# Optimization experiments

Hardware: AMD Instinct MI355X
Metric: run time of the kernel (lower is better)

## Reference

```python
import jax, jax.numpy as jnp
import numpy as np

B, S, D, M = 4, 1024, 128, 20000
THRESH = 0.1          # memory.query_with_indices threshold
CW_MIN = 0.01         # compound_weight > 0.01 gate
TI_MIN = 0.01         # total_influence > 0.01 gate
NORM_EPS = 1e-6       # norm_sq > 1e-6 gate
INF_EPS = 1e-5        # division epsilon


def setup_inputs() -> dict:
    key = jax.random.key(0)
    ks = jax.random.split(key, 4)
    sd = 1.0 / np.sqrt(D)
    return {
        "input_tensor": jax.random.normal(ks[0], (B, S, D), dtype=jnp.float32),
        "mem": jax.random.normal(ks[1], (M, D), dtype=jnp.float32),
        "W1": jax.random.normal(ks[2], (D, D), dtype=jnp.float32) * sd,
        "b1": jnp.zeros((D,), dtype=jnp.float32),
        "ln_g": jnp.ones((D,), dtype=jnp.float32),
        "ln_b": jnp.zeros((D,), dtype=jnp.float32),
        "W2": jax.random.normal(ks[3], (D, D), dtype=jnp.float32) * sd,
        "b2": jnp.zeros((D,), dtype=jnp.float32),
    }


def reference(input_tensor, mem, W1, b1, ln_g, ln_b, W2, b2):
    x = input_tensor  # [B,S,D]
    # fusion_net: Linear -> LayerNorm -> ReLU
    h = jnp.einsum("bsd,ed->bse", x, W1) + b1
    mu = h.mean(-1, keepdims=True)
    var = h.var(-1, keepdims=True)
    h = (h - mu) * jax.lax.rsqrt(var + 1e-5) * ln_g + ln_b
    feats = jax.nn.relu(h)
    raw = jnp.einsum("bsd,ed->bse", feats, W2) + b2  # [B,S,D]

    # GraphMemory query: cosine similarity, keep entries with sim > THRESH
    xn = x * jax.lax.rsqrt(jnp.sum(x * x, -1, keepdims=True) + 1e-12)
    mn = mem * jax.lax.rsqrt(jnp.sum(mem * mem, -1, keepdims=True) + 1e-12)
    sim = jnp.einsum("bsd,md->bsm", xn, mn)              # [B,S,M]
    w = jnp.where(sim > THRESH, sim, 0.0)                # per-token weights

    # compound_weight per batch & memory slot (sum over seq positions)
    cw = w.sum(axis=1)                                   # [B,M]
    norm_sq = jnp.sum(mem * mem, -1)                     # [M]
    active = (cw > CW_MIN) & (norm_sq > NORM_EPS)        # [B,M]
    eff = jnp.where(active, cw, 0.0)                     # effective weights

    # projection of each target vec onto each memory vec
    safe_ns = jnp.where(norm_sq > NORM_EPS, norm_sq, 1.0)
    coef = jnp.einsum("bsd,md->bsm", raw, mem) / safe_ns # [B,S,M]
    correction = jnp.einsum("bsm,bm,md->bsd", coef, eff, mem)  # [B,S,D]

    ti = eff.sum(-1)                                     # [B] total_influence
    corr = correction / (ti + INF_EPS)[:, None, None]
    final = jnp.where((ti > TI_MIN)[:, None, None], raw + 0.5 * corr, raw)
    return final
```

## Files before the change

### kernel.cpp

```cpp
#include <hip/hip_runtime.h>

#define DD 128
#define SS 1024
#define BB 4
#define M_TOT 20000
#define M_PAD 20480
#define GM_NCH 64
#define GM_CH 320
#define FMLP_BLOCKS 128
#define PREP_BLOCKS 320

typedef __bf16 bf16x8 __attribute__((ext_vector_type(8)));
typedef _Float16 f16x8 __attribute__((ext_vector_type(8)));
typedef unsigned short u16x8 __attribute__((ext_vector_type(8)));
typedef float f32x16 __attribute__((ext_vector_type(16)));

union BF8 { bf16x8 b; u16x8 u; };

__device__ __forceinline__ unsigned short f2bf(float f) {
    __bf16 h = (__bf16)f;
    return __builtin_bit_cast(unsigned short, h);
}
__device__ __forceinline__ float bf2f(unsigned short h) {
    return __uint_as_float(((unsigned int)h) << 16);
}

__global__ __launch_bounds__(256) void k_front(
    const float* __restrict__ x, const float* __restrict__ W1,
    const float* __restrict__ b1, const float* __restrict__ ln_g,
    const float* __restrict__ ln_b, const float* __restrict__ W2,
    const float* __restrict__ b2, const float* __restrict__ mem,
    unsigned short* __restrict__ xnb, float* __restrict__ raw,
    unsigned short* __restrict__ mnb, _Float16* __restrict__ mnT,
    float* __restrict__ norm_sq, float* __restrict__ ti,
    float* __restrict__ cw, float* __restrict__ G) {
    __shared__ __align__(16) char smem_raw[64 * 136 * 2];
    const int tid = threadIdx.x;
    const int bid = blockIdx.x;

    if (bid < FMLP_BLOCKS) {
        unsigned short* featsL = (unsigned short*)smem_raw;
        float* redp = (float*)(smem_raw + 8704);
        float2* stats = (float2*)(smem_raw + 8704 + 1024);
        const int lane = tid & 63, wv = tid >> 6;
        const int col = lane & 31, hi = lane >> 5;
        const int t0 = bid * 32;
        const int ct = wv;

        bf16x8 Af[8];
        float sq = 0.f;
        const float* xrow = x + (size_t)(t0 + col) * DD + hi * 8;
        #pragma unroll
        for (int kk = 0; kk < 8; ++kk) {
            float4 p = *(const float4*)(xrow + kk * 16);
            float4 q = *(const float4*)(xrow + kk * 16 + 4);
            BF8 t;
            t.u[0] = f2bf(p.x); t.u[1] = f2bf(p.y); t.u[2] = f2bf(p.z); t.u[3] = f2bf(p.w);
            t.u[4] = f2bf(q.x); t.u[5] = f2bf(q.y); t.u[6] = f2bf(q.z); t.u[7] = f2bf(q.w);
            Af[kk] = t.b;
            sq += p.x * p.x + p.y * p.y + p.z * p.z + p.w * p.w;
            sq += q.x * q.x + q.y * q.y + q.z * q.z + q.w * q.w;
        }
        sq += __shfl_xor(sq, 32);
        float xrs = rsqrtf(sq + 1e-12f);
        if (wv == 0) {
            unsigned short* xo = xnb + (size_t)(t0 + col) * DD + hi * 8;
            #pragma unroll
            for (int kk = 0; kk < 8; ++kk) {
                BF8 t; t.b = Af[kk];
                u16x8 o;
                #pragma unroll
                for (int j = 0; j < 8; ++j) o[j] = f2bf(bf2f(t.u[j]) * xrs);
                *(u16x8*)(xo + kk * 16) = o;
            }
        }

        f32x16 acc;
        {
            float bv = b1[ct * 32 + col];
            #pragma unroll
            for (int r = 0; r < 16; ++r) acc[r] = bv;
        }
        const float* w1row = W1 + (size_t)(ct * 32 + col) * DD + hi * 8;
        #pragma unroll
        for (int kk = 0; kk < 8; ++kk) {
            float4 p = *(const float4*)(w1row + kk * 16);
            float4 q = *(const float4*)(w1row + kk * 16 + 4);
            BF8 t;
            t.u[0] = f2bf(p.x); t.u[1] = f2bf(p.y); t.u[2] = f2bf(p.z); t.u[3] = f2bf(p.w);
            t.u[4] = f2bf(q.x); t.u[5] = f2bf(q.y); t.u[6] = f2bf(q.z); t.u[7] = f2bf(q.w);
            acc = __builtin_amdgcn_mfma_f32_32x32x16_bf16(Af[kk], t.b, acc, 0, 0, 0);
        }

        float rs_[16], rq_[16];
        #pragma unroll
        for (int r = 0; r < 16; ++r) { float v = acc[r]; rs_[r] = v; rq_[r] = v * v; }
        #pragma unroll
        for (int off = 1; off < 32; off <<= 1) {
            #pragma unroll
            for (int r = 0; r < 16; ++r) {
                rs_[r] += __shfl_xor(rs_[r], off);
                rq_[r] += __shfl_xor(rq_[r], off);
            }
        }
        if (col == 0) {
            #pragma unroll
            for (int r = 0; r < 16; ++r) {
                int row = (r & 3) + 8 * (r >> 2) + 4 * hi;
                redp[(wv * 32 + row) * 2 + 0] = rs_[r];
                redp[(wv * 32 + row) * 2 + 1] = rq_[r];
            }
        }
        __syncthreads();
        if (tid < 32) {
            float S = redp[(0 * 32 + tid) * 2] + redp[(1 * 32 + tid) * 2] +
                      redp[(2 * 32 + tid) * 2] + redp[(3 * 32 + tid) * 2];
            float Q = redp[(0 * 32 + tid) * 2 + 1] + redp[(1 * 32 + tid) * 2 + 1] +
                      redp[(2 * 32 + tid) * 2 + 1] + redp[(3 * 32 + tid) * 2 + 1];
            float mu = S * (1.f / 128.f);
            float rstd = rsqrtf(Q * (1.f / 128.f) - mu * mu + 1e-5f);
            stats[tid] = make_float2(mu, rstd);
        }
        __syncthreads();

        {
            float gv = ln_g[ct * 32 + col], bv = ln_b[ct * 32 + col];
            #pragma unroll
            for (int r = 0; r < 16; ++r) {
                int row = (r & 3) + 8 * (r >> 2) + 4 * hi;
                float2 st = stats[row];
                float v = fmaxf((acc[r] - st.x) * st.y * gv + bv, 0.f);
                featsL[row * 136 + ct * 32 + col] = f2bf(v);
            }
        }
        __syncthreads();

        f32x16 a2;
        {
            float bv = b2[ct * 32 + col];
            #pragma unroll
            for (int r = 0; r < 16; ++r) a2[r] = bv;
        }
        const float* w2row = W2 + (size_t)(ct * 32 + col) * DD + hi * 8;
        #pragma unroll
        for (int kk = 0; kk < 8; ++kk) {
            bf16x8 Aq = *(const bf16x8*)&featsL[(lane & 31) * 136 + hi * 8 + kk * 16];
            float4 p = *(const float4*)(w2row + kk * 16);
            float4 q = *(const float4*)(w2row + kk * 16 + 4);
            BF8 t;
            t.u[0] = f2bf(p.x); t.u[1] = f2bf(p.y); t.u[2] = f2bf(p.z); t.u[3] = f2bf(p.w);
            t.u[4] = f2bf(q.x); t.u[5] = f2bf(q.y); t.u[6] = f2bf(q.z); t.u[7] = f2bf(q.w);
            a2 = __builtin_amdgcn_mfma_f32_32x32x16_bf16(Aq, t.b, a2, 0, 0, 0);
        }
        #pragma unroll
        for (int r = 0; r < 16; ++r) {
            int row = (r & 3) + 8 * (r >> 2) + 4 * hi;
            raw[(size_t)(t0 + row) * DD + ct * 32 + col] = a2[r];
        }
    } else {
        unsigned short* RM = (unsigned short*)smem_raw;
        const int pb = bid - FMLP_BLOCKS;
        const int m0 = pb * 64;
        cw[pb * 256 + tid] = 0.0f;
        if (pb < 64) ((float4*)G)[pb * 256 + tid] =
            make_float4(0.f, 0.f, 0.f, 0.f);
        if (pb == 0 && tid < BB) ti[tid] = 0.0f;

        const int r = tid >> 2, seg = tid & 3;
        const int m = m0 + r;
        const bool ok = m < M_TOT;
        float4 v[8];
        const float4* src = (const float4*)mem + (size_t)m * 32 + seg * 8;
        #pragma unroll
        for (int i = 0; i < 8; ++i)
            v[i] = ok ? src[i] : make_float4(0.f, 0.f, 0.f, 0.f);
        float ss = 0.f;
        #pragma unroll
        for (int i = 0; i < 8; ++i)
            ss += v[i].x * v[i].x + v[i].y * v[i].y + v[i].z * v[i].z + v[i].w * v[i].w;
        ss += __shfl_xor(ss, 1);
        ss += __shfl_xor(ss, 2);
        float rs = rsqrtf(ss + 1e-12f);
        if (seg == 0) norm_sq[m] = ss;

        #pragma unroll
        for (int i = 0; i < 4; ++i) {
            float4 a = v[2 * i], bq = v[2 * i + 1];
            u16x8 o;
            o[0] = f2bf(a.x * rs); o[1] = f2bf(a.y * rs);
            o[2] = f2bf(a.z * rs); o[3] = f2bf(a.w * rs);
            o[4] = f2bf(bq.x * rs); o[5] = f2bf(bq.y * rs);
            o[6] = f2bf(bq.z * rs); o[7] = f2bf(bq.w * rs);
            *(u16x8*)(mnb + (size_t)m * DD + seg * 32 + i * 8) = o;
            *(u16x8*)(RM + r * 136 + seg * 32 + i * 8) = o;
        }
        __syncthreads();
        const int d = tid >> 1, half = tid & 1;
        _Float16* dst = mnT + (size_t)d * M_PAD + m0 + half * 32;
        #pragma unroll
        for (int q = 0; q < 4; ++q) {
            f16x8 o;
            #pragma unroll
            for (int j = 0; j < 8; ++j)
                o[j] = (_Float16)bf2f(RM[(half * 32 + q * 8 + j) * 136 + d]);
            *(f16x8*)(dst + q * 8) = o;
        }
    }
}

__global__ __launch_bounds__(256, 3) void k_cw(
    const unsigned short* __restrict__ xnb, const unsigned short* __restrict__ mnb,
    float* __restrict__ cw) {
    __shared__ unsigned short As[4][32 * 128];
    const int tid = threadIdx.x, lane = tid & 63, wv = tid >> 6;
    const int c = lane & 31, h = lane >> 5;
    const int b = blockIdx.z;
    const int mw = blockIdx.x * 256 + wv * 64;
    const int s_base = blockIdx.y * 256;

    const int srow = tid >> 4, sk16 = tid & 15;
    const int soff = srow * 128 + ((sk16 * 8) ^ ((srow & 15) << 3));
    const int srow1 = srow + 16;
    const int soff1 = srow1 * 128 + ((sk16 * 8) ^ ((srow1 & 15) << 3));
    const unsigned short* xbase = xnb + ((size_t)b * SS + s_base) * DD;

    bf16x8 Bf[2][8];
    #pragma unroll
    for (int ct = 0; ct < 2; ++ct)
        #pragma unroll
        for (int kk = 0; kk < 8; ++kk)
            Bf[ct][kk] = *(const bf16x8*)(mnb + (size_t)(mw + ct * 32 + c) * DD +
                                          kk * 16 + h * 8);

    {
        u16x8 a0 = *(const u16x8*)(xbase + (size_t)srow * DD + sk16 * 8);
        u16x8 a1 = *(const u16x8*)(xbase + (size_t)srow1 * DD + sk16 * 8);
        const unsigned short* n1 = xbase + (size_t)32 * DD;
        u16x8 b0 = *(const u16x8*)(n1 + (size_t)srow * DD + sk16 * 8);
        u16x8 b1 = *(const u16x8*)(n1 + (size_t)srow1 * DD + sk16 * 8);
        *(u16x8*)&As[0][soff] = a0; *(u16x8*)&As[0][soff1] = a1;
        *(u16x8*)&As[1][soff] = b0; *(u16x8*)&As[1][soff1] = b1;
    }

    float cw0 = 0.f, cw1 = 0.f;
    #pragma unroll 1
    for (int p = 0; p < 4; ++p) {
        __syncthreads();
        u16x8 w0, w1, w2, w3;
        if (p < 3) {
            const unsigned short* n0 = xbase + (size_t)(2 * p + 2) * 32 * DD;
            const unsigned short* n1 = xbase + (size_t)(2 * p + 3) * 32 * DD;
            w0 = *(const u16x8*)(n0 + (size_t)srow * DD + sk16 * 8);
            w1 = *(const u16x8*)(n0 + (size_t)srow1 * DD + sk16 * 8);
            w2 = *(const u16x8*)(n1 + (size_t)srow * DD + sk16 * 8);
            w3 = *(const u16x8*)(n1 + (size_t)srow1 * DD + sk16 * 8);
        }
        {
            f32x16 p0, p1;
            #pragma unroll
            for (int r = 0; r < 16; ++r) { p0[r] = 0.f; p1[r] = 0.f; }
            const unsigned short* Ab = As[(2 * p) & 3];
            __builtin_amdgcn_s_setprio(1);
            #pragma unroll
            for (int kk = 0; kk < 8; ++kk) {
                bf16x8 Afr = *(const bf16x8*)&Ab[c * 128 + ((kk * 16 + h * 8) ^ ((c & 15) << 3))];
                p0 = __builtin_amdgcn_mfma_f32_32x32x16_bf16(Afr, Bf[0][kk], p0, 0, 0, 0);
                p1 = __builtin_amdgcn_mfma_f32_32x32x16_bf16(Afr, Bf[1][kk], p1, 0, 0, 0);
            }
            __builtin_amdgcn_s_setprio(0);
            #pragma unroll
            for (int r = 0; r < 16; ++r) {
                float a = p0[r], bb = p1[r];
                cw0 += a > 0.1f ? a : 0.f;
                cw1 += bb > 0.1f ? bb : 0.f;
            }
        }
        {
            f32x16 p0, p1;
            #pragma unroll
            for (int r = 0; r < 16; ++r) { p0[r] = 0.f; p1[r] = 0.f; }
            const unsigned short* Ab = As[(2 * p + 1) & 3];
            __builtin_amdgcn_s_setprio(1);
            #pragma unroll
            for (int kk = 0; kk < 8; ++kk) {
                bf16x8 Afr = *(const bf16x8*)&Ab[c * 128 + ((kk * 16 + h * 8) ^ ((c & 15) << 3))];
                p0 = __builtin_amdgcn_mfma_f32_32x32x16_bf16(Afr, Bf[0][kk], p0, 0, 0, 0);
                p1 = __builtin_amdgcn_mfma_f32_32x32x16_bf16(Afr, Bf[1][kk], p1, 0, 0, 0);
            }
            __builtin_amdgcn_s_setprio(0);
            if (p < 3) {
                unsigned short* An0 = As[(2 * p + 2) & 3];
                unsigned short* An1 = As[(2 * p + 3) & 3];
                *(u16x8*)&An0[soff] = w0; *(u16x8*)&An0[soff1] = w1;
                *(u16x8*)&An1[soff] = w2; *(u16x8*)&An1[soff1] = w3;
            }
            #pragma unroll
            for (int r = 0; r < 16; ++r) {
                float a = p0[r], bb = p1[r];
                cw0 += a > 0.1f ? a : 0.f;
                cw1 += bb > 0.1f ? bb : 0.f;
            }
        }
    }
    cw0 += __shfl_xor(cw0, 32);
    cw1 += __shfl_xor(cw1, 32);
    if (lane < 32) {
        atomicAdd(&cw[(size_t)b * M_PAD + mw + c], cw0);
        atomicAdd(&cw[(size_t)b * M_PAD + mw + 32 + c], cw1);
    }
}

__global__ __launch_bounds__(256) void k_gmatm(
    const _Float16* __restrict__ mnT, const float* __restrict__ cw,
    const float* __restrict__ norm_sq, float* __restrict__ ti,
    float* __restrict__ G) {
    __shared__ __align__(16) _Float16 effH[GM_CH];
    __shared__ float rb[4];
    const int tid = threadIdx.x, lane = tid & 63, wv = tid >> 6;
    const int c = lane & 31, h = lane >> 5;
    const int b = blockIdx.y;
    const int m0 = blockIdx.x * GM_CH;

    float tsum = 0.f;
    #pragma unroll
    for (int idx = tid; idx < GM_CH; idx += 256) {
        int m = m0 + idx;
        float e = 0.f;
        if (m < M_TOT) {
            float cc = cw[(size_t)b * M_PAD + m];
            float ns = norm_sq[m];
            e = (cc > 0.01f && ns > 1e-6f) ? cc : 0.f;
        }
        effH[idx] = (_Float16)e;
        tsum += e;
    }
    #pragma unroll
    for (int off = 1; off < 64; off <<= 1) tsum += __shfl_xor(tsum, off);
    if (lane == 0) rb[wv] = tsum;
    __syncthreads();
    if (tid == 0) atomicAdd(&ti[b], rb[0] + rb[1] + rb[2] + rb[3]);

    f32x16 a0, a1, a2, a3;
    #pragma unroll
    for (int r = 0; r < 16; ++r) { a0[r] = 0.f; a1[r] = 0.f; a2[r] = 0.f; a3[r] = 0.f; }

    const _Float16* Arow = mnT + (size_t)(wv * 32 + c) * M_PAD + m0;
    const _Float16* B0r = mnT + (size_t)(0 * 32 + c) * M_PAD + m0;
    const _Float16* B1r = mnT + (size_t)(1 * 32 + c) * M_PAD + m0;
    const _Float16* B2r = mnT + (size_t)(2 * 32 + c) * M_PAD + m0;
    const _Float16* B3r = mnT + (size_t)(3 * 32 + c) * M_PAD + m0;

    #pragma unroll 1
    for (int t = 0; t < GM_CH / 64; ++t) {
        #pragma unroll
        for (int kk = 0; kk < 4; ++kk) {
            const int mo = t * 64 + kk * 16 + h * 8;
            f16x8 au = *(const f16x8*)(Arow + mo);
            f16x8 ef = *(const f16x8*)&effH[mo];
            f16x8 af = au * ef;
            f16x8 B0 = *(const f16x8*)(B0r + mo);
            f16x8 B1 = *(const f16x8*)(B1r + mo);
            f16x8 B2 = *(const f16x8*)(B2r + mo);
            f16x8 B3 = *(const f16x8*)(B3r + mo);
            a0 = __builtin_amdgcn_mfma_f32_32x32x16_f16(af, B0, a0, 0, 0, 0);
            a1 = __builtin_amdgcn_mfma_f32_32x32x16_f16(af, B1, a1, 0, 0, 0);
            a2 = __builtin_amdgcn_mfma_f32_32x32x16_f16(af, B2, a2, 0, 0, 0);
            a3 = __builtin_amdgcn_mfma_f32_32x32x16_f16(af, B3, a3, 0, 0, 0);
        }
    }
    float* Gb = G + (size_t)b * DD * DD;
    #pragma unroll
    for (int r = 0; r < 16; ++r) {
        int rf = (r & 3) + 8 * (r >> 2) + 4 * h;
        atomicAdd(&Gb[(wv * 32 + rf) * DD + 0 * 32 + c], a0[r]);
        atomicAdd(&Gb[(wv * 32 + rf) * DD + 1 * 32 + c], a1[r]);
        atomicAdd(&Gb[(wv * 32 + rf) * DD + 2 * 32 + c], a2[r]);
        atomicAdd(&Gb[(wv * 32 + rf) * DD + 3 * 32 + c], a3[r]);
    }
}

__global__ __launch_bounds__(256) void k_final(
    const float* __restrict__ raw, const float* __restrict__ G,
    const float* __restrict__ ti, float* __restrict__ out) {
    const int tid = threadIdx.x, lane = tid & 63, wv = tid >> 6;
    const int col = lane & 31, hi = lane >> 5;
    const int t0 = blockIdx.x * 32;
    const int b = blockIdx.x >> 5;
    const int ct = wv;

    bf16x8 Af[8];
    const float* rrow = raw + (size_t)(t0 + col) * DD + hi * 8;
    #pragma unroll
    for (int kk = 0; kk < 8; ++kk) {
        float4 p = *(const float4*)(rrow + kk * 16);
        float4 q = *(const float4*)(rrow + kk * 16 + 4);
        BF8 t;
        t.u[0] = f2bf(p.x); t.u[1] = f2bf(p.y); t.u[2] = f2bf(p.z); t.u[3] = f2bf(p.w);
        t.u[4] = f2bf(q.x); t.u[5] = f2bf(q.y); t.u[6] = f2bf(q.z); t.u[7] = f2bf(q.w);
        Af[kk] = t.b;
    }
    f32x16 acc;
    #pragma unroll
    for (int r = 0; r < 16; ++r) acc[r] = 0.f;
    const float* grow = G + (size_t)b * DD * DD + (size_t)(ct * 32 + col) * DD + hi * 8;
    #pragma unroll
    for (int kk = 0; kk < 8; ++kk) {
        float4 p = *(const float4*)(grow + kk * 16);
        float4 q = *(const float4*)(grow + kk * 16 + 4);
        BF8 t;
        t.u[0] = f2bf(p.x); t.u[1] = f2bf(p.y); t.u[2] = f2bf(p.z); t.u[3] = f2bf(p.w);
        t.u[4] = f2bf(q.x); t.u[5] = f2bf(q.y); t.u[6] = f2bf(q.z); t.u[7] = f2bf(q.w);
        acc = __builtin_amdgcn_mfma_f32_32x32x16_bf16(Af[kk], t.b, acc, 0, 0, 0);
    }
    float tib = ti[b];
    float scale = (tib > 0.01f) ? 0.5f / (tib + 1e-5f) : 0.0f;
    #pragma unroll
    for (int r = 0; r < 16; ++r) {
        int row = (r & 3) + 8 * (r >> 2) + 4 * hi;
        size_t idx = (size_t)(t0 + row) * DD + ct * 32 + col;
        out[idx] = raw[idx] + scale * acc[r];
    }
}

extern "C" void kernel_launch(void* const* d_in, const int* in_sizes, int n_in,
                              void* d_out, int out_size, void* d_ws, size_t ws_size,
                              hipStream_t stream) {
    const float* x   = (const float*)d_in[0];
    const float* mem = (const float*)d_in[1];
    const float* W1  = (const float*)d_in[2];
    const float* b1  = (const float*)d_in[3];
    const float* lg  = (const float*)d_in[4];
    const float* lb  = (const float*)d_in[5];
    const float* W2  = (const float*)d_in[6];
    const float* b2  = (const float*)d_in[7];
    float* out = (float*)d_out;

    float* wsf = (float*)d_ws;
    size_t off = 0;
    unsigned short* mnb = (unsigned short*)(wsf + off); off += (size_t)M_PAD * 64;
    _Float16* mnT = (_Float16*)(wsf + off);             off += (size_t)M_PAD * 64;
    float* norm_sq = wsf + off;                         off += M_PAD;
    unsigned short* xnb = (unsigned short*)(wsf + off); off += (size_t)BB * SS * 64;
    float* raw = wsf + off;                             off += (size_t)BB * SS * DD;
    float* cw  = wsf + off;                             off += (size_t)BB * M_PAD;
    float* G   = wsf + off;                             off += (size_t)BB * DD * DD;
    float* ti  = wsf + off;                             off += BB;

    k_front<<<dim3(FMLP_BLOCKS + PREP_BLOCKS), 256, 0, stream>>>(
        x, W1, b1, lg, lb, W2, b2, mem, xnb, raw, mnb, mnT, norm_sq, ti, cw, G);
    k_cw<<<dim3(M_PAD / 256, 4, BB), 256, 0, stream>>>(xnb, mnb, cw);
    k_gmatm<<<dim3(GM_NCH, BB), 256, 0, stream>>>(mnT, cw, norm_sq, ti, G);
    k_final<<<dim3(SS * BB / 32), 256, 0, stream>>>(raw, G, ti, out);
}
```

Baseline: 83.96 us.

## Replace G atomic accumulation with per-chunk partials and a separate reduction kernel

k_gmatm now writes each chunk's 128x128 partial Gram matrix to its own slot instead of issuing float atomics into a shared G. A new kernel k_gmat2 sums the 64 partials per batch and stores G as bf16, so k_final loads bf16 directly without converting. The aim is to remove contention from the atomic adds and the G zero-init in k_front. The cost is an extra launch and about 16 MB of partial-buffer writes and reads.

```diff
diff --git a/kernel.cpp b/kernel.cpp
--- a/kernel.cpp
+++ b/kernel.cpp
@@ -33,7 +33,7 @@
     unsigned short* __restrict__ xnb, float* __restrict__ raw,
     unsigned short* __restrict__ mnb, _Float16* __restrict__ mnT,
     float* __restrict__ norm_sq, float* __restrict__ ti,
-    float* __restrict__ cw, float* __restrict__ G) {
+    float* __restrict__ cw) {
     __shared__ __align__(16) char smem_raw[64 * 136 * 2];
     const int tid = threadIdx.x;
     const int bid = blockIdx.x;
@@ -162,8 +162,6 @@
         const int pb = bid - FMLP_BLOCKS;
         const int m0 = pb * 64;
         cw[pb * 256 + tid] = 0.0f;
-        if (pb < 64) ((float4*)G)[pb * 256 + tid] =
-            make_float4(0.f, 0.f, 0.f, 0.f);
         if (pb == 0 && tid < BB) ti[tid] = 0.0f;
 
         const int r = tid >> 2, seg = tid & 3;
@@ -313,7 +311,7 @@
 __global__ __launch_bounds__(256) void k_gmatm(
     const _Float16* __restrict__ mnT, const float* __restrict__ cw,
     const float* __restrict__ norm_sq, float* __restrict__ ti,
-    float* __restrict__ G) {
+    float* __restrict__ pG) {
     __shared__ __align__(16) _Float16 effH[GM_CH];
     __shared__ float rb[4];
     const int tid = threadIdx.x, lane = tid & 63, wv = tid >> 6;
@@ -368,19 +366,45 @@
             a3 = __builtin_amdgcn_mfma_f32_32x32x16_f16(af, B3, a3, 0, 0, 0);
         }
     }
-    float* Gb = G + (size_t)b * DD * DD;
+    float* o = pG + (size_t)(blockIdx.x * BB + b) * (DD * DD);
     #pragma unroll
     for (int r = 0; r < 16; ++r) {
         int rf = (r & 3) + 8 * (r >> 2) + 4 * h;
-        atomicAdd(&Gb[(wv * 32 + rf) * DD + 0 * 32 + c], a0[r]);
-        atomicAdd(&Gb[(wv * 32 + rf) * DD + 1 * 32 + c], a1[r]);
-        atomicAdd(&Gb[(wv * 32 + rf) * DD + 2 * 32 + c], a2[r]);
-        atomicAdd(&Gb[(wv * 32 + rf) * DD + 3 * 32 + c], a3[r]);
+        o[(wv * 32 + rf) * DD + 0 * 32 + c] = a0[r];
+        o[(wv * 32 + rf) * DD + 1 * 32 + c] = a1[r];
+        o[(wv * 32 + rf) * DD + 2 * 32 + c] = a2[r];
+        o[(wv * 32 + rf) * DD + 3 * 32 + c] = a3[r];
+    }
+}
+
+__global__ __launch_bounds__(256) void k_gmat2(const float* __restrict__ pG,
+                                               unsigned short* __restrict__ Gb) {
+    __shared__ float4 redv[256];
+    const int tid = threadIdx.x;
+    const int b = blockIdx.y;
+    const int f4i = blockIdx.x * 64 + (tid & 63);
+    const int cg = tid >> 6;
+    const float4* pG4 = (const float4*)pG;
+    float4 s = make_float4(0.f, 0.f, 0.f, 0.f);
+    for (int c = cg; c < GM_NCH; c += 4) {
+        float4 p = pG4[(size_t)(c * BB + b) * (DD * DD / 4) + f4i];
+        s.x += p.x; s.y += p.y; s.z += p.z; s.w += p.w;
+    }
+    redv[tid] = s;
+    __syncthreads();
+    if (tid < 64) {
+        float4 r0 = redv[tid], r1 = redv[tid + 64], r2 = redv[tid + 128], r3 = redv[tid + 192];
+        ushort4 o;
+        o.x = f2bf(r0.x + r1.x + r2.x + r3.x);
+        o.y = f2bf(r0.y + r1.y + r2.y + r3.y);
+        o.z = f2bf(r0.z + r1.z + r2.z + r3.z);
+        o.w = f2bf(r0.w + r1.w + r2.w + r3.w);
+        *(ushort4*)&Gb[(size_t)b * (DD * DD) + f4i * 4] = o;
     }
 }
 
 __global__ __launch_bounds__(256) void k_final(
-    const float* __restrict__ raw, const float* __restrict__ G,
+    const float* __restrict__ raw, const unsigned short* __restrict__ Gb,
     const float* __restrict__ ti, float* __restrict__ out) {
     const int tid = threadIdx.x, lane = tid & 63, wv = tid >> 6;
     const int col = lane & 31, hi = lane >> 5;
@@ -402,15 +426,11 @@
     f32x16 acc;
     #pragma unroll
     for (int r = 0; r < 16; ++r) acc[r] = 0.f;
-    const float* grow = G + (size_t)b * DD * DD + (size_t)(ct * 32 + col) * DD + hi * 8;
+    const unsigned short* grow = Gb + (size_t)b * DD * DD + (size_t)(ct * 32 + col) * DD + hi * 8;
     #pragma unroll
     for (int kk = 0; kk < 8; ++kk) {
-        float4 p = *(const float4*)(grow + kk * 16);
-        float4 q = *(const float4*)(grow + kk * 16 + 4);
-        BF8 t;
-        t.u[0] = f2bf(p.x); t.u[1] = f2bf(p.y); t.u[2] = f2bf(p.z); t.u[3] = f2bf(p.w);
-        t.u[4] = f2bf(q.x); t.u[5] = f2bf(q.y); t.u[6] = f2bf(q.z); t.u[7] = f2bf(q.w);
-        acc = __builtin_amdgcn_mfma_f32_32x32x16_bf16(Af[kk], t.b, acc, 0, 0, 0);
+        bf16x8 Bw = *(const bf16x8*)(grow + kk * 16);
+        acc = __builtin_amdgcn_mfma_f32_32x32x16_bf16(Af[kk], Bw, acc, 0, 0, 0);
     }
     float tib = ti[b];
     float scale = (tib > 0.01f) ? 0.5f / (tib + 1e-5f) : 0.0f;
@@ -443,12 +463,14 @@
     unsigned short* xnb = (unsigned short*)(wsf + off); off += (size_t)BB * SS * 64;
     float* raw = wsf + off;                             off += (size_t)BB * SS * DD;
     float* cw  = wsf + off;                             off += (size_t)BB * M_PAD;
-    float* G   = wsf + off;                             off += (size_t)BB * DD * DD;
+    unsigned short* Gb = (unsigned short*)(wsf + off);  off += (size_t)BB * DD * DD / 2;
     float* ti  = wsf + off;                             off += BB;
+    float* pG  = wsf + off;                             off += (size_t)GM_NCH * BB * DD * DD;
 
     k_front<<<dim3(FMLP_BLOCKS + PREP_BLOCKS), 256, 0, stream>>>(
-        x, W1, b1, lg, lb, W2, b2, mem, xnb, raw, mnb, mnT, norm_sq, ti, cw, G);
+        x, W1, b1, lg, lb, W2, b2, mem, xnb, raw, mnb, mnT, norm_sq, ti, cw);
     k_cw<<<dim3(M_PAD / 256, 4, BB), 256, 0, stream>>>(xnb, mnb, cw);
-    k_gmatm<<<dim3(GM_NCH, BB), 256, 0, stream>>>(mnT, cw, norm_sq, ti, G);
-    k_final<<<dim3(SS * BB / 32), 256, 0, stream>>>(raw, G, ti, out);
-}
+    k_gmatm<<<dim3(GM_NCH, BB), 256, 0, stream>>>(mnT, cw, norm_sq, ti, pG);
+    k_gmat2<<<dim3(DD * DD / 256, BB), 256, 0, stream>>>(pG, Gb);
+    k_final<<<dim3(SS * BB / 32), 256, 0, stream>>>(raw, Gb, ti, out);
+}
```

Result: faster. 77.23 us (-8.0%).
